# Performance work log

Hardware: AMD Instinct MI355X
Metric: run time of the kernel (lower is better)

The kernel has to match this reference:

```python
import jax, jax.numpy as jnp
import numpy as np
import math

B, H, S, D = 2, 12, 2048, 64

def setup_inputs() -> dict:
    key = jax.random.key(0)
    kq, kk, kv, km = jax.random.split(key, 4)
    Q = jax.random.normal(kq, (B, H, S, D), dtype=jnp.float32)
    K = jax.random.normal(kk, (B, H, S, D), dtype=jnp.float32)
    V = jax.random.normal(kv, (B, H, S, D), dtype=jnp.float32)
    mask = jax.random.randint(km, (B, 1, S, S), 0, 2, dtype=jnp.int32)
    return {"Q": Q, "K": K, "V": V, "mask": mask}

def reference(Q, K, V, mask):
    d_k = K.shape[-1]
    # [B,H,S,S] scores
    scores = jnp.einsum('bhqd,bhkd->bhqk', Q, K) / math.sqrt(d_k)
    scores = jnp.where(mask == 0, jnp.float32(-1e20), scores)
    attn = jax.nn.softmax(scores, axis=-1)
    # dropout p=0 -> identity
    return jnp.einsum('bhqk,bhkd->bhqd', attn, V)
```

## Files before the change

kernel.cpp:

```cpp
#include <hip/hip_runtime.h>
#include <hip/hip_bf16.h>
#include <math.h>


#define BB 2
#define HH 12
#define SS 2048
#define DD 64
#define BQ 128
#define BK 64
#define GG 2
#define KG (SS / GG)
#define NTG (KG / BK)
#define LP 72
#define LT 76
#define NROWS (BB * HH * SS)
#define QSCALE 0.1803368801111f

typedef __attribute__((ext_vector_type(8))) short bf8_t;
typedef __attribute__((ext_vector_type(4))) short bf4_t;
typedef __attribute__((ext_vector_type(4))) float f4_t;
typedef unsigned long long u64;

__device__ __forceinline__ short f2bf(float f) {
    __hip_bfloat16 h = __float2bfloat16(f);
    return *reinterpret_cast<short*>(&h);
}

__device__ __forceinline__ void gl_lds16(const void* g, void* l) {
    __builtin_amdgcn_global_load_lds(
        (const __attribute__((address_space(1))) unsigned*)(g),
        (__attribute__((address_space(3))) unsigned*)(l), 16, 0, 0);
}

__device__ __forceinline__ bf8_t ldfrag(const unsigned short* buf, int row, int c8) {
    return *(const bf8_t*)&buf[((row << 3) | (c8 ^ (row & 7))) << 3];
}

__global__ __launch_bounds__(256) void prepass(
    const float* __restrict__ V, const float* __restrict__ K,
    const int* __restrict__ M, unsigned short* __restrict__ Vt,
    unsigned short* __restrict__ Kb, u64* __restrict__ Mbt)
{
    __shared__ unsigned short Ts[64][LT];
    const int bx   = blockIdx.x;
    const int tid  = threadIdx.x;
    const int w    = tid >> 6;
    const int lane = tid & 63;
    const int b    = bx >> 11;
    const int row  = bx & 2047;

    {
        const int* src = M + (size_t)bx * SS;
        #pragma unroll
        for (int p = 0; p < 8; ++p) {
            int k = p * 256 + w * 64 + lane;
            u64 bm = __ballot(src[k] != 0);
            if (lane == 0)
                Mbt[(size_t)b * 32 * SS + (size_t)(p * 4 + w) * SS + row] = bm;
        }
    }

    if (bx < 768) {
        const int s0 = (bx & 31) * 64;
        const int bh = bx >> 5;
        const float* Vg = V + (size_t)bh * SS * DD;
        #pragma unroll
        for (int pass = 0; pass < 4; ++pass) {
            int c = tid + pass * 256;
            int r = c >> 4, col = (c & 15) * 4;
            float4 v = *(const float4*)(Vg + (size_t)(s0 + r) * DD + col);
            bf4_t p; p.x = f2bf(v.x); p.y = f2bf(v.y); p.z = f2bf(v.z); p.w = f2bf(v.w);
            *(bf4_t*)&Ts[r][col] = p;
        }
        __syncthreads();
        unsigned short* Vo = Vt + (size_t)bh * DD * SS;
        #pragma unroll
        for (int pass = 0; pass < 2; ++pass) {
            int c = tid + pass * 256;
            int d = c >> 3, sc = (c & 7) * 8;
            unsigned short t[8];
            #pragma unroll
            for (int u = 0; u < 8; ++u) t[u] = Ts[sc + u][d];
            uint4 o;
            o.x = (unsigned)t[0] | ((unsigned)t[1] << 16);
            o.y = (unsigned)t[2] | ((unsigned)t[3] << 16);
            o.z = (unsigned)t[4] | ((unsigned)t[5] << 16);
            o.w = (unsigned)t[6] | ((unsigned)t[7] << 16);
            *(uint4*)(Vo + (size_t)d * SS + s0 + sc) = o;
        }
    } else if (bx < 2304) {
        size_t i = ((size_t)(bx - 768) * 256 + tid) * 8;
        float4 a = *(const float4*)(K + i);
        float4 b2 = *(const float4*)(K + i + 4);
        uint4 o;
        o.x = (unsigned short)f2bf(a.x)  | ((unsigned)(unsigned short)f2bf(a.y)  << 16);
        o.y = (unsigned short)f2bf(a.z)  | ((unsigned)(unsigned short)f2bf(a.w)  << 16);
        o.z = (unsigned short)f2bf(b2.x) | ((unsigned)(unsigned short)f2bf(b2.y) << 16);
        o.w = (unsigned short)f2bf(b2.z) | ((unsigned)(unsigned short)f2bf(b2.w) << 16);
        *(uint4*)(Kb + i) = o;
    }
}

__global__ __launch_bounds__(256, 3) void attn_fwd(
    const float* __restrict__ Q, const unsigned short* __restrict__ Kb,
    const unsigned short* __restrict__ Vt, const u64* __restrict__ Mbt,
    float* __restrict__ Opart, float* __restrict__ Lpart)
{
    __shared__ unsigned short Ks[BK * DD];
    __shared__ unsigned short Vts[DD * BK];
    __shared__ unsigned short Ps[BQ][LP];

    const int tid  = threadIdx.x;
    const int w    = tid >> 6;
    const int lane = tid & 63;
    const int quad = lane >> 4;
    const int l16  = lane & 15;
    const int q0   = blockIdx.x * BQ;
    const int bh   = blockIdx.y;
    const int g    = blockIdx.z;
    const int b    = bh / HH;
    const int qbase = w * 32;

    const float*          Qg  = Q   + (size_t)bh * SS * DD;
    const unsigned short* Kg  = Kb  + (size_t)bh * SS * DD;
    const unsigned short* Vg  = Vt  + (size_t)bh * DD * SS;
    const u64*            Mgt = Mbt + (size_t)b * 32 * SS;
    float* Og = Opart + ((size_t)g * BB * HH + bh) * SS * DD;
    float* Lg = Lpart + (size_t)g * NROWS + (size_t)bh * SS;

    bf8_t bq[2][2];
    #pragma unroll
    for (int qf = 0; qf < 2; ++qf)
        #pragma unroll
        for (int ks = 0; ks < 2; ++ks) {
            const float* qp = Qg + (size_t)(q0 + qbase + qf * 16 + l16) * DD
                                 + ks * 32 + quad * 8;
            float4 x = *(const float4*)qp;
            float4 y = *(const float4*)(qp + 4);
            bf8_t f;
            f[0] = f2bf(x.x * QSCALE); f[1] = f2bf(x.y * QSCALE);
            f[2] = f2bf(x.z * QSCALE); f[3] = f2bf(x.w * QSCALE);
            f[4] = f2bf(y.x * QSCALE); f[5] = f2bf(y.y * QSCALE);
            f[6] = f2bf(y.z * QSCALE); f[7] = f2bf(y.w * QSCALE);
            bq[qf][ks] = f;
        }

    bf8_t onesf;
    {
        short ov = (l16 == 0) ? (short)0x3F80 : (short)0;
        #pragma unroll
        for (int j = 0; j < 8; ++j) onesf[j] = ov;
    }

    f4_t oacc[2][4], lacc[2];
    #pragma unroll
    for (int qf = 0; qf < 2; ++qf) {
        lacc[qf] = (f4_t){0.f, 0.f, 0.f, 0.f};
        #pragma unroll
        for (int nf = 0; nf < 4; ++nf) oacc[qf][nf] = (f4_t){0.f, 0.f, 0.f, 0.f};
    }

    u64 mpf[2];
    #pragma unroll
    for (int qf = 0; qf < 2; ++qf)
        mpf[qf] = Mgt[(size_t)(g * NTG) * SS + q0 + qbase + qf * 16 + l16];

    for (int t = 0; t < NTG; ++t) {
        const int k0 = g * KG + t * BK;
        __syncthreads();
        #pragma unroll
        for (int j = 0; j < 2; ++j) {
            const int bc = (w * 2 + j) * 64;
            const int c  = bc + lane;
            const int r  = c >> 3;
            const int c8 = (c & 7) ^ (r & 7);
            gl_lds16(Kg + (size_t)(k0 + r) * DD + c8 * 8, &Ks[bc * 8]);
            gl_lds16(Vg + (size_t)r * SS + k0 + c8 * 8, &Vts[bc * 8]);
        }
        u64 cm[2] = {mpf[0] >> (quad * 4), mpf[1] >> (quad * 4)};
        __syncthreads();
        if (t + 1 < NTG) {
            #pragma unroll
            for (int qf = 0; qf < 2; ++qf)
                mpf[qf] = Mgt[(size_t)(g * NTG + t + 1) * SS
                              + q0 + qbase + qf * 16 + l16];
        }

        f4_t sacc[4][2];
        #pragma unroll
        for (int kf = 0; kf < 4; ++kf) {
            bf8_t ak0 = ldfrag(Ks, kf * 16 + l16, quad);
            bf8_t ak1 = ldfrag(Ks, kf * 16 + l16, 4 + quad);
            #pragma unroll
            for (int qf = 0; qf < 2; ++qf) {
                f4_t a = (f4_t){0.f, 0.f, 0.f, 0.f};
                a = __builtin_amdgcn_mfma_f32_16x16x32_bf16(ak0, bq[qf][0], a, 0, 0, 0);
                a = __builtin_amdgcn_mfma_f32_16x16x32_bf16(ak1, bq[qf][1], a, 0, 0, 0);
                sacc[kf][qf] = a;
            }
        }

        #pragma unroll
        for (int qf = 0; qf < 2; ++qf) {
            const int prow = qbase + qf * 16 + l16;
            #pragma unroll
            for (int kf = 0; kf < 4; ++kf) {
                bf4_t pk;
                #pragma unroll
                for (int r = 0; r < 4; ++r) {
                    float e = exp2f(sacc[kf][qf][r]);
                    e = ((cm[qf] >> (kf * 16 + r)) & 1ull) ? e : 0.f;
                    pk[r] = f2bf(e);
                }
                *(bf4_t*)&Ps[prow][kf * 16 + quad * 4] = pk;
            }
        }

        bf8_t ap[2][2];
        #pragma unroll
        for (int qf = 0; qf < 2; ++qf) {
            const int prow = qbase + qf * 16 + l16;
            ap[qf][0] = *(const bf8_t*)&Ps[prow][quad * 8];
            ap[qf][1] = *(const bf8_t*)&Ps[prow][32 + quad * 8];
            lacc[qf] = __builtin_amdgcn_mfma_f32_16x16x32_bf16(ap[qf][0], onesf, lacc[qf], 0, 0, 0);
            lacc[qf] = __builtin_amdgcn_mfma_f32_16x16x32_bf16(ap[qf][1], onesf, lacc[qf], 0, 0, 0);
        }

        #pragma unroll
        for (int nf = 0; nf < 4; ++nf) {
            bf8_t bv0 = ldfrag(Vts, nf * 16 + l16, quad);
            bf8_t bv1 = ldfrag(Vts, nf * 16 + l16, 4 + quad);
            #pragma unroll
            for (int qf = 0; qf < 2; ++qf) {
                oacc[qf][nf] = __builtin_amdgcn_mfma_f32_16x16x32_bf16(ap[qf][0], bv0, oacc[qf][nf], 0, 0, 0);
                oacc[qf][nf] = __builtin_amdgcn_mfma_f32_16x16x32_bf16(ap[qf][1], bv1, oacc[qf][nf], 0, 0, 0);
            }
        }
    }

    #pragma unroll
    for (int qf = 0; qf < 2; ++qf) {
        #pragma unroll
        for (int r = 0; r < 4; ++r) {
            const int row = q0 + qbase + qf * 16 + quad * 4 + r;
            #pragma unroll
            for (int nf = 0; nf < 4; ++nf)
                Og[(size_t)row * DD + nf * 16 + l16] = oacc[qf][nf][r];
        }
        if (l16 == 0) {
            #pragma unroll
            for (int r = 0; r < 4; ++r)
                Lg[q0 + qbase + qf * 16 + quad * 4 + r] = lacc[qf][r];
        }
    }
}

__global__ __launch_bounds__(256) void reduce_o(
    const float* __restrict__ Opart, const float* __restrict__ Lpart,
    float* __restrict__ O)
{
    const size_t idx = (size_t)blockIdx.x * 256 + threadIdx.x;
    const size_t row = idx >> 4;
    const int    c   = (int)(idx & 15) * 4;
    const float* p0 = Opart + row * DD + c;
    const float* p1 = p0 + (size_t)NROWS * DD;
    float4 a = *(const float4*)p0;
    float4 b = *(const float4*)p1;
    const float inv = 1.f / (Lpart[row] + Lpart[NROWS + row]);
    float4 o;
    o.x = (a.x + b.x) * inv;
    o.y = (a.y + b.y) * inv;
    o.z = (a.z + b.z) * inv;
    o.w = (a.w + b.w) * inv;
    *(float4*)(O + row * DD + c) = o;
}

extern "C" void kernel_launch(void* const* d_in, const int* in_sizes, int n_in,
                              void* d_out, int out_size, void* d_ws, size_t ws_size,
                              hipStream_t stream) {
    const float* Q = (const float*)d_in[0];
    const float* K = (const float*)d_in[1];
    const float* V = (const float*)d_in[2];
    const int*   M = (const int*)d_in[3];
    float*       O = (float*)d_out;

    unsigned short* Vt = (unsigned short*)d_ws;
    unsigned short* Kb = Vt + (size_t)BB * HH * SS * DD;
    u64*            Mbt = (u64*)(Kb + (size_t)BB * HH * SS * DD);
    float*          Opart = (float*)(Mbt + (size_t)BB * 32 * SS);
    float*          Lpart = Opart + (size_t)GG * NROWS * DD;

    prepass<<<dim3(BB * SS), 256, 0, stream>>>(V, K, M, Vt, Kb, Mbt);
    attn_fwd<<<dim3(SS / BQ, BB * HH, GG), 256, 0, stream>>>(Q, Kb, Vt, Mbt,
                                                             Opart, Lpart);
    reduce_o<<<dim3((NROWS * DD / 4) / 256), 256, 0, stream>>>(Opart, Lpart, O);
}
```

Measured before the change: 168.1 us.

## Merge key-split halves into one 512-thread block with in-LDS reduction

The two key-range splits, previously separate blocks writing partial O and L to global memory, now run as two 4-wave groups inside one 512-thread block. Each group stages its own K/V tiles in a shared LDS buffer, and the partial results are combined through LDS at the end. This drops the separate reduce kernel and the global round trip of the partial outputs. Source pointers are also precomputed and advanced each step instead of recomputing addresses. The cost is a larger LDS footprint per block (about 70 KB) and fewer, larger blocks, which may reduce how many blocks fit on a CU.

New measurement: 187.8 us. 11.7% more time.

```diff
diff --git a/kernel.cpp b/kernel.cpp
--- a/kernel.cpp
+++ b/kernel.cpp
@@ -12,10 +12,14 @@
 #define GG 2
 #define KG (SS / GG)
 #define NTG (KG / BK)
-#define LP 72
 #define LT 76
-#define NROWS (BB * HH * SS)
 #define QSCALE 0.1803368801111f
+
+#define TILE_B   8192
+#define PS_OFF   33280
+#define LP       72
+#define LF_OFF   70144
+#define LDS_B    70656
 
 typedef __attribute__((ext_vector_type(8))) short bf8_t;
 typedef __attribute__((ext_vector_type(4))) short bf4_t;
@@ -102,32 +106,35 @@
     }
 }
 
-__global__ __launch_bounds__(256, 3) void attn_fwd(
+__global__ __launch_bounds__(512, 4) void attn_fwd(
     const float* __restrict__ Q, const unsigned short* __restrict__ Kb,
     const unsigned short* __restrict__ Vt, const u64* __restrict__ Mbt,
-    float* __restrict__ Opart, float* __restrict__ Lpart)
+    float* __restrict__ O)
 {
-    __shared__ unsigned short Ks[BK * DD];
-    __shared__ unsigned short Vts[DD * BK];
-    __shared__ unsigned short Ps[BQ][LP];
+    __shared__ __align__(16) char ls[LDS_B];
 
     const int tid  = threadIdx.x;
     const int w    = tid >> 6;
+    const int g    = w >> 2;
+    const int wl   = w & 3;
     const int lane = tid & 63;
     const int quad = lane >> 4;
     const int l16  = lane & 15;
     const int q0   = blockIdx.x * BQ;
     const int bh   = blockIdx.y;
-    const int g    = blockIdx.z;
     const int b    = bh / HH;
-    const int qbase = w * 32;
-
-    const float*          Qg  = Q   + (size_t)bh * SS * DD;
-    const unsigned short* Kg  = Kb  + (size_t)bh * SS * DD;
-    const unsigned short* Vg  = Vt  + (size_t)bh * DD * SS;
-    const u64*            Mgt = Mbt + (size_t)b * 32 * SS;
-    float* Og = Opart + ((size_t)g * BB * HH + bh) * SS * DD;
-    float* Lg = Lpart + (size_t)g * NROWS + (size_t)bh * SS;
+    const int qbase = wl * 32;
+
+    unsigned short* tileK = (unsigned short*)(ls + g * 2 * TILE_B);
+    unsigned short* tileV = (unsigned short*)(ls + g * 2 * TILE_B + TILE_B);
+    unsigned short* Ps    = (unsigned short*)(ls + PS_OFF);
+    float*          Of    = (float*)ls;
+    float*          Lf    = (float*)(ls + LF_OFF);
+
+    const float*          Qg = Q  + (size_t)bh * SS * DD;
+    const unsigned short* Kg = Kb + (size_t)bh * SS * DD;
+    const unsigned short* Vg = Vt + (size_t)bh * DD * SS;
+    float*                Og = O  + (size_t)bh * SS * DD;
 
     bf8_t bq[2][2];
     #pragma unroll
@@ -161,37 +168,54 @@
         for (int nf = 0; nf < 4; ++nf) oacc[qf][nf] = (f4_t){0.f, 0.f, 0.f, 0.f};
     }
 
+    const unsigned short* kSrc[2];
+    const unsigned short* vSrc[2];
+    unsigned short*       kDst[2];
+    unsigned short*       vDst[2];
+    #pragma unroll
+    for (int j = 0; j < 2; ++j) {
+        const int bc = (wl * 2 + j) * 64;
+        const int c  = bc + lane;
+        const int r  = c >> 3;
+        const int c8 = (c & 7) ^ (r & 7);
+        kSrc[j] = Kg + (size_t)(g * KG + r) * DD + c8 * 8;
+        vSrc[j] = Vg + (size_t)r * SS + g * KG + c8 * 8;
+        kDst[j] = tileK + bc * 8;
+        vDst[j] = tileV + bc * 8;
+    }
+    const u64* mp[2];
     u64 mpf[2];
     #pragma unroll
-    for (int qf = 0; qf < 2; ++qf)
-        mpf[qf] = Mgt[(size_t)(g * NTG) * SS + q0 + qbase + qf * 16 + l16];
+    for (int qf = 0; qf < 2; ++qf) {
+        mp[qf] = Mbt + (size_t)b * 32 * SS + (size_t)(g * NTG) * SS
+                     + q0 + qbase + qf * 16 + l16;
+        mpf[qf] = *mp[qf];
+    }
 
     for (int t = 0; t < NTG; ++t) {
-        const int k0 = g * KG + t * BK;
         __syncthreads();
         #pragma unroll
         for (int j = 0; j < 2; ++j) {
-            const int bc = (w * 2 + j) * 64;
-            const int c  = bc + lane;
-            const int r  = c >> 3;
-            const int c8 = (c & 7) ^ (r & 7);
-            gl_lds16(Kg + (size_t)(k0 + r) * DD + c8 * 8, &Ks[bc * 8]);
-            gl_lds16(Vg + (size_t)r * SS + k0 + c8 * 8, &Vts[bc * 8]);
+            gl_lds16(kSrc[j], kDst[j]);
+            gl_lds16(vSrc[j], vDst[j]);
+            kSrc[j] += BK * DD;
+            vSrc[j] += BK;
         }
         u64 cm[2] = {mpf[0] >> (quad * 4), mpf[1] >> (quad * 4)};
         __syncthreads();
         if (t + 1 < NTG) {
             #pragma unroll
-            for (int qf = 0; qf < 2; ++qf)
-                mpf[qf] = Mgt[(size_t)(g * NTG + t + 1) * SS
-                              + q0 + qbase + qf * 16 + l16];
+            for (int qf = 0; qf < 2; ++qf) {
+                mp[qf] += SS;
+                mpf[qf] = *mp[qf];
+            }
         }
 
         f4_t sacc[4][2];
         #pragma unroll
         for (int kf = 0; kf < 4; ++kf) {
-            bf8_t ak0 = ldfrag(Ks, kf * 16 + l16, quad);
-            bf8_t ak1 = ldfrag(Ks, kf * 16 + l16, 4 + quad);
+            bf8_t ak0 = ldfrag(tileK, kf * 16 + l16, quad);
+            bf8_t ak1 = ldfrag(tileK, kf * 16 + l16, 4 + quad);
             #pragma unroll
             for (int qf = 0; qf < 2; ++qf) {
                 f4_t a = (f4_t){0.f, 0.f, 0.f, 0.f};
@@ -203,7 +227,7 @@
 
         #pragma unroll
         for (int qf = 0; qf < 2; ++qf) {
-            const int prow = qbase + qf * 16 + l16;
+            const int prow = w * 32 + qf * 16 + l16;
             #pragma unroll
             for (int kf = 0; kf < 4; ++kf) {
                 bf4_t pk;
@@ -213,24 +237,24 @@
                     e = ((cm[qf] >> (kf * 16 + r)) & 1ull) ? e : 0.f;
                     pk[r] = f2bf(e);
                 }
-                *(bf4_t*)&Ps[prow][kf * 16 + quad * 4] = pk;
+                *(bf4_t*)&Ps[prow * LP + kf * 16 + quad * 4] = pk;
             }
         }
 
         bf8_t ap[2][2];
         #pragma unroll
         for (int qf = 0; qf < 2; ++qf) {
-            const int prow = qbase + qf * 16 + l16;
-            ap[qf][0] = *(const bf8_t*)&Ps[prow][quad * 8];
-            ap[qf][1] = *(const bf8_t*)&Ps[prow][32 + quad * 8];
+            const int prow = w * 32 + qf * 16 + l16;
+            ap[qf][0] = *(const bf8_t*)&Ps[prow * LP + quad * 8];
+            ap[qf][1] = *(const bf8_t*)&Ps[prow * LP + 32 + quad * 8];
             lacc[qf] = __builtin_amdgcn_mfma_f32_16x16x32_bf16(ap[qf][0], onesf, lacc[qf], 0, 0, 0);
             lacc[qf] = __builtin_amdgcn_mfma_f32_16x16x32_bf16(ap[qf][1], onesf, lacc[qf], 0, 0, 0);
         }
 
         #pragma unroll
         for (int nf = 0; nf < 4; ++nf) {
-            bf8_t bv0 = ldfrag(Vts, nf * 16 + l16, quad);
-            bf8_t bv1 = ldfrag(Vts, nf * 16 + l16, 4 + quad);
+            bf8_t bv0 = ldfrag(tileV, nf * 16 + l16, quad);
+            bf8_t bv1 = ldfrag(tileV, nf * 16 + l16, 4 + quad);
             #pragma unroll
             for (int qf = 0; qf < 2; ++qf) {
                 oacc[qf][nf] = __builtin_amdgcn_mfma_f32_16x16x32_bf16(ap[qf][0], bv0, oacc[qf][nf], 0, 0, 0);
@@ -239,41 +263,39 @@
         }
     }
 
-    #pragma unroll
-    for (int qf = 0; qf < 2; ++qf) {
-        #pragma unroll
-        for (int r = 0; r < 4; ++r) {
-            const int row = q0 + qbase + qf * 16 + quad * 4 + r;
-            #pragma unroll
-            for (int nf = 0; nf < 4; ++nf)
-                Og[(size_t)row * DD + nf * 16 + l16] = oacc[qf][nf][r];
-        }
-        if (l16 == 0) {
-            #pragma unroll
-            for (int r = 0; r < 4; ++r)
-                Lg[q0 + qbase + qf * 16 + quad * 4 + r] = lacc[qf][r];
-        }
-    }
-}
-
-__global__ __launch_bounds__(256) void reduce_o(
-    const float* __restrict__ Opart, const float* __restrict__ Lpart,
-    float* __restrict__ O)
-{
-    const size_t idx = (size_t)blockIdx.x * 256 + threadIdx.x;
-    const size_t row = idx >> 4;
-    const int    c   = (int)(idx & 15) * 4;
-    const float* p0 = Opart + row * DD + c;
-    const float* p1 = p0 + (size_t)NROWS * DD;
-    float4 a = *(const float4*)p0;
-    float4 b = *(const float4*)p1;
-    const float inv = 1.f / (Lpart[row] + Lpart[NROWS + row]);
-    float4 o;
-    o.x = (a.x + b.x) * inv;
-    o.y = (a.y + b.y) * inv;
-    o.z = (a.z + b.z) * inv;
-    o.w = (a.w + b.w) * inv;
-    *(float4*)(O + row * DD + c) = o;
+    __syncthreads();
+    if (g == 1) {
+        #pragma unroll
+        for (int qf = 0; qf < 2; ++qf) {
+            #pragma unroll
+            for (int r = 0; r < 4; ++r) {
+                const int row = qbase + qf * 16 + quad * 4 + r;
+                #pragma unroll
+                for (int nf = 0; nf < 4; ++nf)
+                    Of[row * 65 + nf * 16 + l16] = oacc[qf][nf][r];
+            }
+            if (l16 == 0) {
+                #pragma unroll
+                for (int r = 0; r < 4; ++r)
+                    Lf[qbase + qf * 16 + quad * 4 + r] = lacc[qf][r];
+            }
+        }
+    }
+    __syncthreads();
+    if (g == 0) {
+        #pragma unroll
+        for (int qf = 0; qf < 2; ++qf)
+            #pragma unroll
+            for (int r = 0; r < 4; ++r) {
+                const int row = qbase + qf * 16 + quad * 4 + r;
+                const float l0 = __shfl(lacc[qf][r], lane & 48);
+                const float inv = 1.f / (l0 + Lf[row]);
+                #pragma unroll
+                for (int nf = 0; nf < 4; ++nf)
+                    Og[(size_t)(q0 + row) * DD + nf * 16 + l16] =
+                        (oacc[qf][nf][r] + Of[row * 65 + nf * 16 + l16]) * inv;
+            }
+    }
 }
 
 extern "C" void kernel_launch(void* const* d_in, const int* in_sizes, int n_in,
@@ -285,14 +307,10 @@
     const int*   M = (const int*)d_in[3];
     float*       O = (float*)d_out;
 
-    unsigned short* Vt = (unsigned short*)d_ws;
-    unsigned short* Kb = Vt + (size_t)BB * HH * SS * DD;
+    unsigned short* Vt  = (unsigned short*)d_ws;
+    unsigned short* Kb  = Vt + (size_t)BB * HH * SS * DD;
     u64*            Mbt = (u64*)(Kb + (size_t)BB * HH * SS * DD);
-    float*          Opart = (float*)(Mbt + (size_t)BB * 32 * SS);
-    float*          Lpart = Opart + (size_t)GG * NROWS * DD;
 
     prepass<<<dim3(BB * SS), 256, 0, stream>>>(V, K, M, Vt, Kb, Mbt);
-    attn_fwd<<<dim3(SS / BQ, BB * HH, GG), 256, 0, stream>>>(Q, Kb, Vt, Mbt,
-                                                             Opart, Lpart);
-    reduce_o<<<dim3((NROWS * DD / 4) / 256), 256, 0, stream>>>(Opart, Lpart, O);
-}
+    attn_fwd<<<dim3(SS / BQ, BB * HH), 512, 0, stream>>>(Q, Kb, Vt, Mbt, O);
+}
```

## Split keys four ways and process P in half-tiles to shrink LDS

Applied to the files above, without the earlier changes.

Raises the key-dimension split from 2 to 4 groups, so the attention grid gets twice as many blocks, and generalizes the reduction kernel to sum GG partials. The P tile is now built and consumed in two 32-key halves, which shrinks the Ps LDS buffer so occupancy can rise to 4 blocks per SM. Global load addresses are precomputed and advanced by pointer increments. The trade-off is more partial-output traffic to write and reduce, plus tighter register limits under the higher launch bound.

After: 171.8 us. 2.2% more time.

```diff
diff --git a/kernel.cpp b/kernel.cpp
--- a/kernel.cpp
+++ b/kernel.cpp
@@ -9,10 +9,10 @@
 #define DD 64
 #define BQ 128
 #define BK 64
-#define GG 2
+#define GG 4
 #define KG (SS / GG)
 #define NTG (KG / BK)
-#define LP 72
+#define LPH 40
 #define LT 76
 #define NROWS (BB * HH * SS)
 #define QSCALE 0.1803368801111f
@@ -102,14 +102,14 @@
     }
 }
 
-__global__ __launch_bounds__(256, 3) void attn_fwd(
+__global__ __launch_bounds__(256, 4) void attn_fwd(
     const float* __restrict__ Q, const unsigned short* __restrict__ Kb,
     const unsigned short* __restrict__ Vt, const u64* __restrict__ Mbt,
     float* __restrict__ Opart, float* __restrict__ Lpart)
 {
     __shared__ unsigned short Ks[BK * DD];
     __shared__ unsigned short Vts[DD * BK];
-    __shared__ unsigned short Ps[BQ][LP];
+    __shared__ unsigned short Ps[BQ * LPH];
 
     const int tid  = threadIdx.x;
     const int w    = tid >> 6;
@@ -122,10 +122,9 @@
     const int b    = bh / HH;
     const int qbase = w * 32;
 
-    const float*          Qg  = Q   + (size_t)bh * SS * DD;
-    const unsigned short* Kg  = Kb  + (size_t)bh * SS * DD;
-    const unsigned short* Vg  = Vt  + (size_t)bh * DD * SS;
-    const u64*            Mgt = Mbt + (size_t)b * 32 * SS;
+    const float*          Qg = Q  + (size_t)bh * SS * DD;
+    const unsigned short* Kg = Kb + (size_t)bh * SS * DD;
+    const unsigned short* Vg = Vt + (size_t)bh * DD * SS;
     float* Og = Opart + ((size_t)g * BB * HH + bh) * SS * DD;
     float* Lg = Lpart + (size_t)g * NROWS + (size_t)bh * SS;
 
@@ -161,80 +160,87 @@
         for (int nf = 0; nf < 4; ++nf) oacc[qf][nf] = (f4_t){0.f, 0.f, 0.f, 0.f};
     }
 
+    const unsigned short* kSrc[2];
+    const unsigned short* vSrc[2];
+    unsigned short*       kDst[2];
+    unsigned short*       vDst[2];
+    #pragma unroll
+    for (int j = 0; j < 2; ++j) {
+        const int bc = (w * 2 + j) * 64;
+        const int c  = bc + lane;
+        const int r  = c >> 3;
+        const int c8 = (c & 7) ^ (r & 7);
+        kSrc[j] = Kg + (size_t)(g * KG + r) * DD + c8 * 8;
+        vSrc[j] = Vg + (size_t)r * SS + g * KG + c8 * 8;
+        kDst[j] = Ks  + bc * 8;
+        vDst[j] = Vts + bc * 8;
+    }
+    const u64* mp[2];
     u64 mpf[2];
     #pragma unroll
-    for (int qf = 0; qf < 2; ++qf)
-        mpf[qf] = Mgt[(size_t)(g * NTG) * SS + q0 + qbase + qf * 16 + l16];
+    for (int qf = 0; qf < 2; ++qf) {
+        mp[qf] = Mbt + (size_t)b * 32 * SS + (size_t)(g * NTG) * SS
+                     + q0 + qbase + qf * 16 + l16;
+        mpf[qf] = *mp[qf];
+    }
 
     for (int t = 0; t < NTG; ++t) {
-        const int k0 = g * KG + t * BK;
         __syncthreads();
         #pragma unroll
         for (int j = 0; j < 2; ++j) {
-            const int bc = (w * 2 + j) * 64;
-            const int c  = bc + lane;
-            const int r  = c >> 3;
-            const int c8 = (c & 7) ^ (r & 7);
-            gl_lds16(Kg + (size_t)(k0 + r) * DD + c8 * 8, &Ks[bc * 8]);
-            gl_lds16(Vg + (size_t)r * SS + k0 + c8 * 8, &Vts[bc * 8]);
-        }
-        u64 cm[2] = {mpf[0] >> (quad * 4), mpf[1] >> (quad * 4)};
+            gl_lds16(kSrc[j], kDst[j]);
+            gl_lds16(vSrc[j], vDst[j]);
+            kSrc[j] += BK * DD;
+            vSrc[j] += BK;
+        }
+        const u64 cm[2] = {mpf[0] >> (quad * 4), mpf[1] >> (quad * 4)};
         __syncthreads();
         if (t + 1 < NTG) {
             #pragma unroll
-            for (int qf = 0; qf < 2; ++qf)
-                mpf[qf] = Mgt[(size_t)(g * NTG + t + 1) * SS
-                              + q0 + qbase + qf * 16 + l16];
-        }
-
-        f4_t sacc[4][2];
-        #pragma unroll
-        for (int kf = 0; kf < 4; ++kf) {
-            bf8_t ak0 = ldfrag(Ks, kf * 16 + l16, quad);
-            bf8_t ak1 = ldfrag(Ks, kf * 16 + l16, 4 + quad);
-            #pragma unroll
             for (int qf = 0; qf < 2; ++qf) {
-                f4_t a = (f4_t){0.f, 0.f, 0.f, 0.f};
-                a = __builtin_amdgcn_mfma_f32_16x16x32_bf16(ak0, bq[qf][0], a, 0, 0, 0);
-                a = __builtin_amdgcn_mfma_f32_16x16x32_bf16(ak1, bq[qf][1], a, 0, 0, 0);
-                sacc[kf][qf] = a;
+                mp[qf] += SS;
+                mpf[qf] = *mp[qf];
             }
         }
 
         #pragma unroll
-        for (int qf = 0; qf < 2; ++qf) {
-            const int prow = qbase + qf * 16 + l16;
-            #pragma unroll
-            for (int kf = 0; kf < 4; ++kf) {
-                bf4_t pk;
+        for (int h = 0; h < 2; ++h) {
+            #pragma unroll
+            for (int kfh = 0; kfh < 2; ++kfh) {
+                const int kf = h * 2 + kfh;
+                bf8_t ak0 = ldfrag(Ks, kf * 16 + l16, quad);
+                bf8_t ak1 = ldfrag(Ks, kf * 16 + l16, 4 + quad);
                 #pragma unroll
-                for (int r = 0; r < 4; ++r) {
-                    float e = exp2f(sacc[kf][qf][r]);
-                    e = ((cm[qf] >> (kf * 16 + r)) & 1ull) ? e : 0.f;
-                    pk[r] = f2bf(e);
+                for (int qf = 0; qf < 2; ++qf) {
+                    f4_t s = (f4_t){0.f, 0.f, 0.f, 0.f};
+                    s = __builtin_amdgcn_mfma_f32_16x16x32_bf16(ak0, bq[qf][0], s, 0, 0, 0);
+                    s = __builtin_amdgcn_mfma_f32_16x16x32_bf16(ak1, bq[qf][1], s, 0, 0, 0);
+                    bf4_t pk;
+                    #pragma unroll
+                    for (int r = 0; r < 4; ++r) {
+                        float e = exp2f(s[r]);
+                        e = ((cm[qf] >> (kf * 16 + r)) & 1ull) ? e : 0.f;
+                        pk[r] = f2bf(e);
+                    }
+                    *(bf4_t*)&Ps[(qbase + qf * 16 + l16) * LPH
+                                 + kfh * 16 + quad * 4] = pk;
                 }
-                *(bf4_t*)&Ps[prow][kf * 16 + quad * 4] = pk;
             }
-        }
-
-        bf8_t ap[2][2];
-        #pragma unroll
-        for (int qf = 0; qf < 2; ++qf) {
-            const int prow = qbase + qf * 16 + l16;
-            ap[qf][0] = *(const bf8_t*)&Ps[prow][quad * 8];
-            ap[qf][1] = *(const bf8_t*)&Ps[prow][32 + quad * 8];
-            lacc[qf] = __builtin_amdgcn_mfma_f32_16x16x32_bf16(ap[qf][0], onesf, lacc[qf], 0, 0, 0);
-            lacc[qf] = __builtin_amdgcn_mfma_f32_16x16x32_bf16(ap[qf][1], onesf, lacc[qf], 0, 0, 0);
-        }
-
-        #pragma unroll
-        for (int nf = 0; nf < 4; ++nf) {
-            bf8_t bv0 = ldfrag(Vts, nf * 16 + l16, quad);
-            bf8_t bv1 = ldfrag(Vts, nf * 16 + l16, 4 + quad);
+            bf8_t ap[2];
             #pragma unroll
             for (int qf = 0; qf < 2; ++qf) {
-                oacc[qf][nf] = __builtin_amdgcn_mfma_f32_16x16x32_bf16(ap[qf][0], bv0, oacc[qf][nf], 0, 0, 0);
-                oacc[qf][nf] = __builtin_amdgcn_mfma_f32_16x16x32_bf16(ap[qf][1], bv1, oacc[qf][nf], 0, 0, 0);
+                ap[qf] = *(const bf8_t*)&Ps[(qbase + qf * 16 + l16) * LPH
+                                            + quad * 8];
+                lacc[qf] = __builtin_amdgcn_mfma_f32_16x16x32_bf16(
+                    ap[qf], onesf, lacc[qf], 0, 0, 0);
+            }
+            #pragma unroll
+            for (int nf = 0; nf < 4; ++nf) {
+                bf8_t bv = ldfrag(Vts, nf * 16 + l16, h * 4 + quad);
+                #pragma unroll
+                for (int qf = 0; qf < 2; ++qf)
+                    oacc[qf][nf] = __builtin_amdgcn_mfma_f32_16x16x32_bf16(
+                        ap[qf], bv, oacc[qf][nf], 0, 0, 0);
             }
         }
     }
@@ -263,16 +269,17 @@
     const size_t idx = (size_t)blockIdx.x * 256 + threadIdx.x;
     const size_t row = idx >> 4;
     const int    c   = (int)(idx & 15) * 4;
-    const float* p0 = Opart + row * DD + c;
-    const float* p1 = p0 + (size_t)NROWS * DD;
-    float4 a = *(const float4*)p0;
-    float4 b = *(const float4*)p1;
-    const float inv = 1.f / (Lpart[row] + Lpart[NROWS + row]);
+    float4 acc = {0.f, 0.f, 0.f, 0.f};
+    float  l   = 0.f;
+    #pragma unroll
+    for (int g = 0; g < GG; ++g) {
+        float4 a = *(const float4*)(Opart + ((size_t)g * NROWS + row) * DD + c);
+        acc.x += a.x; acc.y += a.y; acc.z += a.z; acc.w += a.w;
+        l += Lpart[(size_t)g * NROWS + row];
+    }
+    const float inv = 1.f / l;
     float4 o;
-    o.x = (a.x + b.x) * inv;
-    o.y = (a.y + b.y) * inv;
-    o.z = (a.z + b.z) * inv;
-    o.w = (a.w + b.w) * inv;
+    o.x = acc.x * inv; o.y = acc.y * inv; o.z = acc.z * inv; o.w = acc.w * inv;
     *(float4*)(O + row * DD + c) = o;
 }
 
@@ -285,9 +292,9 @@
     const int*   M = (const int*)d_in[3];
     float*       O = (float*)d_out;
 
-    unsigned short* Vt = (unsigned short*)d_ws;
-    unsigned short* Kb = Vt + (size_t)BB * HH * SS * DD;
-    u64*            Mbt = (u64*)(Kb + (size_t)BB * HH * SS * DD);
+    unsigned short* Vt    = (unsigned short*)d_ws;
+    unsigned short* Kb    = Vt + (size_t)BB * HH * SS * DD;
+    u64*            Mbt   = (u64*)(Kb + (size_t)BB * HH * SS * DD);
     float*          Opart = (float*)(Mbt + (size_t)BB * 32 * SS);
     float*          Lpart = Opart + (size_t)GG * NROWS * DD;
 
```
